# Optimization experiments

Measured on AMD Instinct MI355X. Metric: run time of the kernel, lower is better.

The kernel has to match this reference:

```python
import jax, jax.numpy as jnp
import numpy as np

N = 50000      # n_nodes
E = 800000     # n_edges (avg degree 16)
D_IN, D_HID, D_OUT = 128, 128, 64


def setup_inputs() -> dict:
    key = jax.random.key(0)
    ks = jax.random.split(key, 6)
    x = jax.random.normal(ks[0], (N, D_IN), dtype=jnp.float32)
    edge_index = jax.random.randint(ks[1], (2, E), 0, N, dtype=jnp.int32)
    # GCNConv params (glorot-ish scale), bias enabled by default in PyG
    W1 = jax.random.normal(ks[2], (D_IN, D_HID), dtype=jnp.float32) * (1.0 / np.sqrt(D_IN))
    b1 = jnp.zeros((D_HID,), dtype=jnp.float32)
    W2 = jax.random.normal(ks[3], (D_HID, D_OUT), dtype=jnp.float32) * (1.0 / np.sqrt(D_HID))
    b2 = jnp.zeros((D_OUT,), dtype=jnp.float32)
    return {"x": x, "edge_index": edge_index, "W1": W1, "b1": b1, "W2": W2, "b2": b2}


def _gcn_conv(x, src, dst, W, b):
    """PyG GCNConv: linear transform, add self-loops (weight 1),
    symmetric D^-1/2 A D^-1/2 aggregation (source->target), add bias."""
    xw = x @ W                                                # [N, Dout]
    ones = jnp.ones(dst.shape[0], dtype=xw.dtype)
    deg = jax.ops.segment_sum(ones, dst, num_segments=N) + 1.0  # +1 self-loop
    dis = jax.lax.rsqrt(deg)                                  # deg >= 1
    norm = dis[src] * dis[dst]                                # [E]
    msg = xw[src] * norm[:, None]                             # gather + scale
    agg = jax.ops.segment_sum(msg, dst, num_segments=N)       # scatter-add
    agg = agg + xw * (dis * dis)[:, None]                     # self-loop term
    return agg + b


def reference(x, edge_index, W1, b1, W2, b2):
    src, dst = edge_index[0], edge_index[1]
    z = jax.nn.relu(_gcn_conv(x, src, dst, W1, b1))
    z = _gcn_conv(z, src, dst, W2, b2)
    return z
```

## Files before the change

### kernel.cpp

```cpp
#include <hip/hip_runtime.h>

#define NN 50000
#define NE 800000
#define NB 196
#define BCAP 4608
#define KPAD 136
#define WSLAB (2 * 64 * KPAD)

typedef __bf16 bf16x8 __attribute__((ext_vector_type(8)));
typedef float  f32x4  __attribute__((ext_vector_type(4)));

static __device__ __forceinline__ float bf2f(unsigned short h){
  union { unsigned u; float f; } c; c.u = ((unsigned)h) << 16; return c.f;
}
static __device__ __forceinline__ unsigned short f2bf(float f){
  union { float f; unsigned u; } c; c.f = f;
  unsigned u = c.u;
  return (unsigned short)((u + 0x7fffu + ((u >> 16) & 1u)) >> 16);
}
static __device__ __forceinline__ void split8(const float* f, bf16x8& hi, bf16x8& lo){
  #pragma unroll
  for (int j = 0; j < 8; j++){
    __bf16 h = (__bf16)f[j];
    hi[j] = h;
    lo[j] = (__bf16)(f[j] - (float)h);
  }
}
static __device__ __forceinline__ void addu4(float* a, uint4 w){
  a[0] += bf2f((unsigned short)(w.x & 0xffffu)); a[1] += bf2f((unsigned short)(w.x >> 16));
  a[2] += bf2f((unsigned short)(w.y & 0xffffu)); a[3] += bf2f((unsigned short)(w.y >> 16));
  a[4] += bf2f((unsigned short)(w.z & 0xffffu)); a[5] += bf2f((unsigned short)(w.z >> 16));
  a[6] += bf2f((unsigned short)(w.w & 0xffffu)); a[7] += bf2f((unsigned short)(w.w >> 16));
}

__global__ __launch_bounds__(256) void k_prep(const float* __restrict__ W1,
    const float* __restrict__ W2, unsigned short* __restrict__ wbuf,
    int* __restrict__ gcur){
  int s = blockIdx.x;
  if (s == 3){
    if (threadIdx.x < NB) gcur[threadIdx.x] = 0;
    return;
  }
  const float* W = (s < 2) ? W1 : W2;
  int ldw = (s < 2) ? 128 : 64;
  int coff = (s == 1) ? 64 : 0;
  unsigned short* wh = wbuf + (size_t)s * WSLAB;
  unsigned short* wl = wh + 64 * KPAD;
  for (int i = threadIdx.x; i < 128 * 64; i += 256){
    int k = i >> 6, n = i & 63;
    float v = W[(size_t)k * ldw + coff + n];
    unsigned short h = f2bf(v);
    unsigned short l = f2bf(v - bf2f(h));
    wh[n * KPAD + k] = h;
    wl[n * KPAD + k] = l;
  }
}

__global__ __launch_bounds__(256) void k_bfill(const int* __restrict__ src,
    const int* __restrict__ dst, int* __restrict__ gcur, unsigned* __restrict__ stg){
  __shared__ int lcnt[NB];
  __shared__ int gbase[NB];
  for (int i = threadIdx.x; i < NB; i += 256) lcnt[i] = 0;
  __syncthreads();
  int per = (NE + gridDim.x - 1) / gridDim.x;
  int e0 = blockIdx.x * per, e1 = min(e0 + per, NE);
  for (int e = e0 + threadIdx.x; e < e1; e += 256)
    atomicAdd(&lcnt[dst[e] >> 8], 1);
  __syncthreads();
  for (int b = threadIdx.x; b < NB; b += 256){
    gbase[b] = atomicAdd(&gcur[b], lcnt[b]);
    lcnt[b] = 0;
  }
  __syncthreads();
  for (int e = e0 + threadIdx.x; e < e1; e += 256){
    int d = dst[e];
    int b = d >> 8;
    unsigned entry = (unsigned)src[e] | (((unsigned)d & 255u) << 16);
    int pos = gbase[b] + atomicAdd(&lcnt[b], 1);
    if (pos < BCAP) stg[(size_t)b * BCAP + pos] = entry;
  }
}

__global__ __launch_bounds__(256) void k_build(const unsigned* __restrict__ stg,
    const int* __restrict__ gcur, int* __restrict__ rowstart, int* __restrict__ cnt,
    float* __restrict__ dis, int* __restrict__ csr){
  __shared__ int lcnt[256];
  __shared__ int sm[256];
  const int b = blockIdx.x;
  const int t = threadIdx.x;
  const int ecnt = min(gcur[b], BCAP);
  const int ebase = b * BCAP;
  lcnt[t] = 0;
  __syncthreads();
  for (int i = t; i < ecnt; i += 256){
    unsigned en = stg[ebase + i];
    atomicAdd(&lcnt[(en >> 16) & 255u], 1);
  }
  __syncthreads();
  int v = lcnt[t];
  sm[t] = v;
  __syncthreads();
  #pragma unroll
  for (int off = 1; off < 256; off <<= 1){
    int x = (t >= off) ? sm[t - off] : 0;
    __syncthreads();
    sm[t] += x;
    __syncthreads();
  }
  const int loff = sm[t] - v;
  const int node = (b << 8) + t;
  if (node < NN){
    rowstart[node] = ebase + loff;
    cnt[node] = v;
    dis[node] = rsqrtf((float)v + 1.0f);
  }
  __syncthreads();
  lcnt[t] = loff;
  __syncthreads();
  for (int i = t; i < ecnt; i += 256){
    unsigned en = stg[ebase + i];
    int pos = atomicAdd(&lcnt[(en >> 16) & 255u], 1);
    csr[ebase + pos] = (int)(en & 0xffffu);
  }
}

__global__ __launch_bounds__(256) void k_gemm1(const float* __restrict__ X,
    const unsigned short* __restrict__ wbuf, const float* __restrict__ dis,
    unsigned short* __restrict__ Y){
  const int t = threadIdx.x;
  const int wv = t >> 6;
  const int lane = t & 63;
  const int m = lane & 15;
  const int quad = lane >> 4;
  const int R0 = blockIdx.x * 64;
  const int row = R0 + wv * 16 + m;
  const int rowc = min(row, NN - 1);
  const float* pX = X + (size_t)rowc * 128 + quad * 8;

  f32x4 acc[8];
  #pragma unroll
  for (int tt = 0; tt < 8; tt++) acc[tt] = (f32x4){0.f, 0.f, 0.f, 0.f};

  #pragma unroll
  for (int ki = 0; ki < 4; ki++){
    float a[8];
    *(float4*)(a)     = *(const float4*)(pX + ki * 32);
    *(float4*)(a + 4) = *(const float4*)(pX + ki * 32 + 4);
    bf16x8 ah, al;
    split8(a, ah, al);
    #pragma unroll
    for (int tt = 0; tt < 8; tt++){
      const unsigned short* bp = wbuf + (tt >> 2) * WSLAB
                               + ((tt & 3) * 16 + m) * KPAD + ki * 32 + quad * 8;
      bf16x8 bh = *(const bf16x8*)bp;
      bf16x8 bl = *(const bf16x8*)(bp + 64 * KPAD);
      acc[tt] = __builtin_amdgcn_mfma_f32_16x16x32_bf16(ah, bh, acc[tt], 0, 0, 0);
      acc[tt] = __builtin_amdgcn_mfma_f32_16x16x32_bf16(ah, bl, acc[tt], 0, 0, 0);
      acc[tt] = __builtin_amdgcn_mfma_f32_16x16x32_bf16(al, bh, acc[tt], 0, 0, 0);
    }
  }

  const int orow = R0 + wv * 16 + quad * 4;
  #pragma unroll
  for (int r = 0; r < 4; r++){
    int gr = orow + r;
    if (gr < NN){
      float dsc = dis[gr];
      #pragma unroll
      for (int tt = 0; tt < 8; tt++)
        Y[(size_t)gr * 128 + (tt >> 2) * 64 + (tt & 3) * 16 + m] = f2bf(acc[tt][r] * dsc);
    }
  }
}

__global__ __launch_bounds__(256) void k_gemm2(const unsigned short* __restrict__ Ah,
    const unsigned short* __restrict__ Al, const unsigned short* __restrict__ Wsl,
    const float* __restrict__ dis, unsigned short* __restrict__ Y){
  const int t = threadIdx.x;
  const int wv = t >> 6;
  const int lane = t & 63;
  const int m = lane & 15;
  const int quad = lane >> 4;
  const int R0 = blockIdx.x * 64;
  const int row = R0 + wv * 16 + m;
  const int rowc = min(row, NN - 1);
  const unsigned short* pAh = Ah + (size_t)rowc * 128 + quad * 8;
  const unsigned short* pAl = Al + (size_t)rowc * 128 + quad * 8;

  f32x4 acc[4];
  #pragma unroll
  for (int tt = 0; tt < 4; tt++) acc[tt] = (f32x4){0.f, 0.f, 0.f, 0.f};

  #pragma unroll
  for (int ki = 0; ki < 4; ki++){
    bf16x8 ah = *(const bf16x8*)(pAh + ki * 32);
    bf16x8 al = *(const bf16x8*)(pAl + ki * 32);
    #pragma unroll
    for (int tt = 0; tt < 4; tt++){
      const unsigned short* bp = Wsl + (tt * 16 + m) * KPAD + ki * 32 + quad * 8;
      bf16x8 bh = *(const bf16x8*)bp;
      bf16x8 bl = *(const bf16x8*)(bp + 64 * KPAD);
      acc[tt] = __builtin_amdgcn_mfma_f32_16x16x32_bf16(ah, bh, acc[tt], 0, 0, 0);
      acc[tt] = __builtin_amdgcn_mfma_f32_16x16x32_bf16(ah, bl, acc[tt], 0, 0, 0);
      acc[tt] = __builtin_amdgcn_mfma_f32_16x16x32_bf16(al, bh, acc[tt], 0, 0, 0);
    }
  }

  const int orow = R0 + wv * 16 + quad * 4;
  #pragma unroll
  for (int r = 0; r < 4; r++){
    int gr = orow + r;
    if (gr < NN){
      float dsc = dis[gr];
      #pragma unroll
      for (int tt = 0; tt < 4; tt++)
        Y[(size_t)gr * 64 + tt * 16 + m] = f2bf(acc[tt][r] * dsc);
    }
  }
}

__global__ __launch_bounds__(256) void k_agg1(const unsigned short* __restrict__ Y,
    const int* __restrict__ rowstart, const int* __restrict__ cnt,
    const int* __restrict__ csr, const float* __restrict__ dis,
    const float* __restrict__ bias, unsigned short* __restrict__ OH,
    unsigned short* __restrict__ OL){
  const int n = (blockIdx.x * 256 + threadIdx.x) >> 6;
  const int lane = threadIdx.x & 63;
  const int q = lane >> 4;
  const int l = lane & 15;
  if (n >= NN) return;
  float a[8] = {0.f, 0.f, 0.f, 0.f, 0.f, 0.f, 0.f, 0.f};
  if (q == 0)
    addu4(a, *(const uint4*)(Y + (size_t)n * 128 + (l << 3)));
  const int start = rowstart[n];
  const int end = start + cnt[n];
  int i = start;
  for (; i + 8 <= end; i += 8){
    int s0 = csr[i + q], s1 = csr[i + 4 + q];
    uint4 w0 = *(const uint4*)(Y + (size_t)s0 * 128 + (l << 3));
    uint4 w1 = *(const uint4*)(Y + (size_t)s1 * 128 + (l << 3));
    addu4(a, w0);
    addu4(a, w1);
  }
  for (; i < end; i += 4){
    int idx = i + q;
    if (idx < end){
      int s = csr[idx];
      addu4(a, *(const uint4*)(Y + (size_t)s * 128 + (l << 3)));
    }
  }
  #pragma unroll
  for (int j = 0; j < 8; j++){
    a[j] += __shfl_xor(a[j], 16);
    a[j] += __shfl_xor(a[j], 32);
  }
  if (q == 0){
    const float dn = dis[n];
    float bi[8];
    *(float4*)(bi)     = *(const float4*)(bias + (l << 3));
    *(float4*)(bi + 4) = *(const float4*)(bias + (l << 3) + 4);
    unsigned hv[4], lv[4];
    #pragma unroll
    for (int j = 0; j < 4; j++){
      float o0 = fmaxf(dn * a[2 * j]     + bi[2 * j],     0.f);
      float o1 = fmaxf(dn * a[2 * j + 1] + bi[2 * j + 1], 0.f);
      unsigned short h0 = f2bf(o0), h1 = f2bf(o1);
      hv[j] = (unsigned)h0 | ((unsigned)h1 << 16);
      lv[j] = (unsigned)f2bf(o0 - bf2f(h0)) | ((unsigned)f2bf(o1 - bf2f(h1)) << 16);
    }
    *(uint4*)(OH + (size_t)n * 128 + (l << 3)) = make_uint4(hv[0], hv[1], hv[2], hv[3]);
    *(uint4*)(OL + (size_t)n * 128 + (l << 3)) = make_uint4(lv[0], lv[1], lv[2], lv[3]);
  }
}

__global__ __launch_bounds__(256) void k_agg64(const unsigned short* __restrict__ Y,
    const int* __restrict__ rowstart, const int* __restrict__ cnt,
    const int* __restrict__ csr, const float* __restrict__ dis,
    const float* __restrict__ bias, float* __restrict__ OUT){
  const int n = (blockIdx.x * 256 + threadIdx.x) >> 6;
  const int lane = threadIdx.x & 63;
  const int q = lane >> 4;
  const int l = lane & 15;
  if (n >= NN) return;
  float a0 = 0.f, a1 = 0.f, a2 = 0.f, a3 = 0.f;
  if (q == 0){
    uint2 w = *(const uint2*)(Y + (size_t)n * 64 + (l << 2));
    a0 = bf2f((unsigned short)(w.x & 0xffffu)); a1 = bf2f((unsigned short)(w.x >> 16));
    a2 = bf2f((unsigned short)(w.y & 0xffffu)); a3 = bf2f((unsigned short)(w.y >> 16));
  }
  const int start = rowstart[n];
  const int end = start + cnt[n];
  int i = start;
  for (; i + 8 <= end; i += 8){
    int s0 = csr[i + q], s1 = csr[i + 4 + q];
    uint2 w0 = *(const uint2*)(Y + (size_t)s0 * 64 + (l << 2));
    uint2 w1 = *(const uint2*)(Y + (size_t)s1 * 64 + (l << 2));
    a0 += bf2f((unsigned short)(w0.x & 0xffffu)) + bf2f((unsigned short)(w1.x & 0xffffu));
    a1 += bf2f((unsigned short)(w0.x >> 16))     + bf2f((unsigned short)(w1.x >> 16));
    a2 += bf2f((unsigned short)(w0.y & 0xffffu)) + bf2f((unsigned short)(w1.y & 0xffffu));
    a3 += bf2f((unsigned short)(w0.y >> 16))     + bf2f((unsigned short)(w1.y >> 16));
  }
  for (; i < end; i += 4){
    int idx = i + q;
    if (idx < end){
      int s = csr[idx];
      uint2 w = *(const uint2*)(Y + (size_t)s * 64 + (l << 2));
      a0 += bf2f((unsigned short)(w.x & 0xffffu)); a1 += bf2f((unsigned short)(w.x >> 16));
      a2 += bf2f((unsigned short)(w.y & 0xffffu)); a3 += bf2f((unsigned short)(w.y >> 16));
    }
  }
  a0 += __shfl_xor(a0, 16); a0 += __shfl_xor(a0, 32);
  a1 += __shfl_xor(a1, 16); a1 += __shfl_xor(a1, 32);
  a2 += __shfl_xor(a2, 16); a2 += __shfl_xor(a2, 32);
  a3 += __shfl_xor(a3, 16); a3 += __shfl_xor(a3, 32);
  if (q == 0){
    const float dn = dis[n];
    float4 bi = *(const float4*)(bias + (l << 2));
    float4 o;
    o.x = dn * a0 + bi.x;
    o.y = dn * a1 + bi.y;
    o.z = dn * a2 + bi.z;
    o.w = dn * a3 + bi.w;
    *(float4*)(OUT + (size_t)n * 64 + (l << 2)) = o;
  }
}

extern "C" void kernel_launch(void* const* d_in, const int* in_sizes, int n_in,
                              void* d_out, int out_size, void* d_ws, size_t ws_size,
                              hipStream_t stream) {
  const float* x  = (const float*)d_in[0];
  const int*   ei = (const int*)d_in[1];
  const int*   src = ei;
  const int*   dst = ei + NE;
  const float* W1 = (const float*)d_in[2];
  const float* b1 = (const float*)d_in[3];
  const float* W2 = (const float*)d_in[4];
  const float* b2 = (const float*)d_in[5];
  float* out = (float*)d_out;

  char* w = (char*)d_ws;
  auto alloc = [&](size_t bytes){ void* p = (void*)w; w += (bytes + 255) & ~(size_t)255; return p; };
  int*   gcur     = (int*)alloc(NB * 4);
  int*   rowstart = (int*)alloc((size_t)NN * 4);
  int*   cnt      = (int*)alloc((size_t)NN * 4);
  float* dis      = (float*)alloc((size_t)NN * 4);
  unsigned* stg   = (unsigned*)alloc((size_t)NB * BCAP * 4);
  int*   csr      = (int*)alloc((size_t)NB * BCAP * 4);
  unsigned short* y1 = (unsigned short*)alloc((size_t)NN * 128 * 2);
  unsigned short* hh = (unsigned short*)alloc((size_t)NN * 128 * 2);
  unsigned short* hl = (unsigned short*)alloc((size_t)NN * 128 * 2);
  unsigned short* y2 = (unsigned short*)alloc((size_t)NN * 64 * 2);
  unsigned short* wbuf = (unsigned short*)alloc((size_t)3 * WSLAB * 2);

  const int CHUNKS = (NN + 63) / 64;
  const int AGG_BLOCKS = (NN * 64 + 255) / 256;

  k_prep <<<4, 256, 0, stream>>>(W1, W2, wbuf, gcur);
  k_bfill<<<256, 256, 0, stream>>>(src, dst, gcur, stg);
  k_build<<<NB, 256, 0, stream>>>(stg, gcur, rowstart, cnt, dis, csr);

  k_gemm1<<<CHUNKS, 256, 0, stream>>>(x, wbuf, dis, y1);
  k_agg1 <<<AGG_BLOCKS, 256, 0, stream>>>(y1, rowstart, cnt, csr, dis, b1, hh, hl);
  k_gemm2<<<CHUNKS, 256, 0, stream>>>(hh, hl, wbuf + (size_t)2 * WSLAB, dis, y2);
  k_agg64<<<AGG_BLOCKS, 256, 0, stream>>>(y2, rowstart, cnt, csr, dis, b2, out);
}
```

Measured before the change: 218.2 us.

## Drop low-part activation split in layer-2 GEMM, widen aggregation gathers

The hidden activations are now stored only as bf16 high parts. This removes the low-part buffer write in agg1, its read in gemm2, and one of the three MFMAs per tile in gemm2, at some cost in precision. agg1 gains a 16-edge unrolled loop for more memory-level parallelism. agg64 now uses 8-lane groups loading 16-byte vectors, so eight edges are in flight per pass instead of four.

```diff
diff --git a/kernel.cpp b/kernel.cpp
--- a/kernel.cpp
+++ b/kernel.cpp
@@ -6,6 +6,7 @@
 #define BCAP 4608
 #define KPAD 136
 #define WSLAB (2 * 64 * KPAD)
+#define CHUNKS 782
 
 typedef __bf16 bf16x8 __attribute__((ext_vector_type(8)));
 typedef float  f32x4  __attribute__((ext_vector_type(4)));
@@ -174,8 +175,8 @@
 }
 
 __global__ __launch_bounds__(256) void k_gemm2(const unsigned short* __restrict__ Ah,
-    const unsigned short* __restrict__ Al, const unsigned short* __restrict__ Wsl,
-    const float* __restrict__ dis, unsigned short* __restrict__ Y){
+    const unsigned short* __restrict__ Wsl, const float* __restrict__ dis,
+    unsigned short* __restrict__ Y){
   const int t = threadIdx.x;
   const int wv = t >> 6;
   const int lane = t & 63;
@@ -185,7 +186,6 @@
   const int row = R0 + wv * 16 + m;
   const int rowc = min(row, NN - 1);
   const unsigned short* pAh = Ah + (size_t)rowc * 128 + quad * 8;
-  const unsigned short* pAl = Al + (size_t)rowc * 128 + quad * 8;
 
   f32x4 acc[4];
   #pragma unroll
@@ -194,7 +194,6 @@
   #pragma unroll
   for (int ki = 0; ki < 4; ki++){
     bf16x8 ah = *(const bf16x8*)(pAh + ki * 32);
-    bf16x8 al = *(const bf16x8*)(pAl + ki * 32);
     #pragma unroll
     for (int tt = 0; tt < 4; tt++){
       const unsigned short* bp = Wsl + (tt * 16 + m) * KPAD + ki * 32 + quad * 8;
@@ -202,7 +201,6 @@
       bf16x8 bl = *(const bf16x8*)(bp + 64 * KPAD);
       acc[tt] = __builtin_amdgcn_mfma_f32_16x16x32_bf16(ah, bh, acc[tt], 0, 0, 0);
       acc[tt] = __builtin_amdgcn_mfma_f32_16x16x32_bf16(ah, bl, acc[tt], 0, 0, 0);
-      acc[tt] = __builtin_amdgcn_mfma_f32_16x16x32_bf16(al, bh, acc[tt], 0, 0, 0);
     }
   }
 
@@ -222,8 +220,7 @@
 __global__ __launch_bounds__(256) void k_agg1(const unsigned short* __restrict__ Y,
     const int* __restrict__ rowstart, const int* __restrict__ cnt,
     const int* __restrict__ csr, const float* __restrict__ dis,
-    const float* __restrict__ bias, unsigned short* __restrict__ OH,
-    unsigned short* __restrict__ OL){
+    const float* __restrict__ bias, unsigned short* __restrict__ OH){
   const int n = (blockIdx.x * 256 + threadIdx.x) >> 6;
   const int lane = threadIdx.x & 63;
   const int q = lane >> 4;
@@ -235,12 +232,20 @@
   const int start = rowstart[n];
   const int end = start + cnt[n];
   int i = start;
+  for (; i + 16 <= end; i += 16){
+    int s0 = csr[i + q],     s1 = csr[i + 4 + q];
+    int s2 = csr[i + 8 + q], s3 = csr[i + 12 + q];
+    uint4 w0 = *(const uint4*)(Y + (size_t)s0 * 128 + (l << 3));
+    uint4 w1 = *(const uint4*)(Y + (size_t)s1 * 128 + (l << 3));
+    uint4 w2 = *(const uint4*)(Y + (size_t)s2 * 128 + (l << 3));
+    uint4 w3 = *(const uint4*)(Y + (size_t)s3 * 128 + (l << 3));
+    addu4(a, w0); addu4(a, w1); addu4(a, w2); addu4(a, w3);
+  }
   for (; i + 8 <= end; i += 8){
     int s0 = csr[i + q], s1 = csr[i + 4 + q];
     uint4 w0 = *(const uint4*)(Y + (size_t)s0 * 128 + (l << 3));
     uint4 w1 = *(const uint4*)(Y + (size_t)s1 * 128 + (l << 3));
-    addu4(a, w0);
-    addu4(a, w1);
+    addu4(a, w0); addu4(a, w1);
   }
   for (; i < end; i += 4){
     int idx = i + q;
@@ -259,17 +264,14 @@
     float bi[8];
     *(float4*)(bi)     = *(const float4*)(bias + (l << 3));
     *(float4*)(bi + 4) = *(const float4*)(bias + (l << 3) + 4);
-    unsigned hv[4], lv[4];
+    unsigned hv[4];
     #pragma unroll
     for (int j = 0; j < 4; j++){
       float o0 = fmaxf(dn * a[2 * j]     + bi[2 * j],     0.f);
       float o1 = fmaxf(dn * a[2 * j + 1] + bi[2 * j + 1], 0.f);
-      unsigned short h0 = f2bf(o0), h1 = f2bf(o1);
-      hv[j] = (unsigned)h0 | ((unsigned)h1 << 16);
-      lv[j] = (unsigned)f2bf(o0 - bf2f(h0)) | ((unsigned)f2bf(o1 - bf2f(h1)) << 16);
+      hv[j] = (unsigned)f2bf(o0) | ((unsigned)f2bf(o1) << 16);
     }
     *(uint4*)(OH + (size_t)n * 128 + (l << 3)) = make_uint4(hv[0], hv[1], hv[2], hv[3]);
-    *(uint4*)(OL + (size_t)n * 128 + (l << 3)) = make_uint4(lv[0], lv[1], lv[2], lv[3]);
   }
 }
 
@@ -279,49 +281,46 @@
     const float* __restrict__ bias, float* __restrict__ OUT){
   const int n = (blockIdx.x * 256 + threadIdx.x) >> 6;
   const int lane = threadIdx.x & 63;
-  const int q = lane >> 4;
-  const int l = lane & 15;
+  const int g = lane >> 3;
+  const int l = lane & 7;
   if (n >= NN) return;
-  float a0 = 0.f, a1 = 0.f, a2 = 0.f, a3 = 0.f;
-  if (q == 0){
-    uint2 w = *(const uint2*)(Y + (size_t)n * 64 + (l << 2));
-    a0 = bf2f((unsigned short)(w.x & 0xffffu)); a1 = bf2f((unsigned short)(w.x >> 16));
-    a2 = bf2f((unsigned short)(w.y & 0xffffu)); a3 = bf2f((unsigned short)(w.y >> 16));
-  }
+  float a[8] = {0.f, 0.f, 0.f, 0.f, 0.f, 0.f, 0.f, 0.f};
+  if (g == 0)
+    addu4(a, *(const uint4*)(Y + (size_t)n * 64 + (l << 3)));
   const int start = rowstart[n];
   const int end = start + cnt[n];
   int i = start;
-  for (; i + 8 <= end; i += 8){
-    int s0 = csr[i + q], s1 = csr[i + 4 + q];
-    uint2 w0 = *(const uint2*)(Y + (size_t)s0 * 64 + (l << 2));
-    uint2 w1 = *(const uint2*)(Y + (size_t)s1 * 64 + (l << 2));
-    a0 += bf2f((unsigned short)(w0.x & 0xffffu)) + bf2f((unsigned short)(w1.x & 0xffffu));
-    a1 += bf2f((unsigned short)(w0.x >> 16))     + bf2f((unsigned short)(w1.x >> 16));
-    a2 += bf2f((unsigned short)(w0.y & 0xffffu)) + bf2f((unsigned short)(w1.y & 0xffffu));
-    a3 += bf2f((unsigned short)(w0.y >> 16))     + bf2f((unsigned short)(w1.y >> 16));
-  }
-  for (; i < end; i += 4){
-    int idx = i + q;
+  for (; i + 16 <= end; i += 16){
+    int s0 = csr[i + g], s1 = csr[i + 8 + g];
+    uint4 w0 = *(const uint4*)(Y + (size_t)s0 * 64 + (l << 3));
+    uint4 w1 = *(const uint4*)(Y + (size_t)s1 * 64 + (l << 3));
+    addu4(a, w0); addu4(a, w1);
+  }
+  for (; i < end; i += 8){
+    int idx = i + g;
     if (idx < end){
       int s = csr[idx];
-      uint2 w = *(const uint2*)(Y + (size_t)s * 64 + (l << 2));
-      a0 += bf2f((unsigned short)(w.x & 0xffffu)); a1 += bf2f((unsigned short)(w.x >> 16));
-      a2 += bf2f((unsigned short)(w.y & 0xffffu)); a3 += bf2f((unsigned short)(w.y >> 16));
-    }
-  }
-  a0 += __shfl_xor(a0, 16); a0 += __shfl_xor(a0, 32);
-  a1 += __shfl_xor(a1, 16); a1 += __shfl_xor(a1, 32);
-  a2 += __shfl_xor(a2, 16); a2 += __shfl_xor(a2, 32);
-  a3 += __shfl_xor(a3, 16); a3 += __shfl_xor(a3, 32);
-  if (q == 0){
+      addu4(a, *(const uint4*)(Y + (size_t)s * 64 + (l << 3)));
+    }
+  }
+  #pragma unroll
+  for (int j = 0; j < 8; j++){
+    a[j] += __shfl_xor(a[j], 8);
+    a[j] += __shfl_xor(a[j], 16);
+    a[j] += __shfl_xor(a[j], 32);
+  }
+  if (g == 0){
     const float dn = dis[n];
-    float4 bi = *(const float4*)(bias + (l << 2));
-    float4 o;
-    o.x = dn * a0 + bi.x;
-    o.y = dn * a1 + bi.y;
-    o.z = dn * a2 + bi.z;
-    o.w = dn * a3 + bi.w;
-    *(float4*)(OUT + (size_t)n * 64 + (l << 2)) = o;
+    float bi[8];
+    *(float4*)(bi)     = *(const float4*)(bias + (l << 3));
+    *(float4*)(bi + 4) = *(const float4*)(bias + (l << 3) + 4);
+    float4 o0, o1;
+    o0.x = dn * a[0] + bi[0]; o0.y = dn * a[1] + bi[1];
+    o0.z = dn * a[2] + bi[2]; o0.w = dn * a[3] + bi[3];
+    o1.x = dn * a[4] + bi[4]; o1.y = dn * a[5] + bi[5];
+    o1.z = dn * a[6] + bi[6]; o1.w = dn * a[7] + bi[7];
+    *(float4*)(OUT + (size_t)n * 64 + (l << 3))     = o0;
+    *(float4*)(OUT + (size_t)n * 64 + (l << 3) + 4) = o1;
   }
 }
 
@@ -348,19 +347,18 @@
   int*   csr      = (int*)alloc((size_t)NB * BCAP * 4);
   unsigned short* y1 = (unsigned short*)alloc((size_t)NN * 128 * 2);
   unsigned short* hh = (unsigned short*)alloc((size_t)NN * 128 * 2);
-  unsigned short* hl = (unsigned short*)alloc((size_t)NN * 128 * 2);
   unsigned short* y2 = (unsigned short*)alloc((size_t)NN * 64 * 2);
   unsigned short* wbuf = (unsigned short*)alloc((size_t)3 * WSLAB * 2);
 
-  const int CHUNKS = (NN + 63) / 64;
   const int AGG_BLOCKS = (NN * 64 + 255) / 256;
+  unsigned short* wsl2 = wbuf + (size_t)2 * WSLAB;
 
   k_prep <<<4, 256, 0, stream>>>(W1, W2, wbuf, gcur);
   k_bfill<<<256, 256, 0, stream>>>(src, dst, gcur, stg);
   k_build<<<NB, 256, 0, stream>>>(stg, gcur, rowstart, cnt, dis, csr);
 
   k_gemm1<<<CHUNKS, 256, 0, stream>>>(x, wbuf, dis, y1);
-  k_agg1 <<<AGG_BLOCKS, 256, 0, stream>>>(y1, rowstart, cnt, csr, dis, b1, hh, hl);
-  k_gemm2<<<CHUNKS, 256, 0, stream>>>(hh, hl, wbuf + (size_t)2 * WSLAB, dis, y2);
+  k_agg1 <<<AGG_BLOCKS, 256, 0, stream>>>(y1, rowstart, cnt, csr, dis, b1, hh);
+  k_gemm2<<<CHUNKS, 256, 0, stream>>>(hh, wsl2, dis, y2);
   k_agg64<<<AGG_BLOCKS, 256, 0, stream>>>(y2, rowstart, cnt, csr, dis, b2, out);
 }
```

New measurement: 212.2 us. -2.7%, faster.
